# Performance work log

Hardware: AMD Instinct MI355X
Metric: run time of the kernel (lower is better)

Reference implementation:

```python
import jax, jax.numpy as jnp
import numpy as np

KS = 3        # kernel_size
DIL = 2       # dilation
HEAD_DIM = 32


def _unfold(x, ks, dil):
    """torch nn.Unfold(ks, dilation=dil, padding=dil*(ks-1)//2, stride=1).
    x: [B, C, H, W] -> [B, C, ks*ks, H, W] (channel-major patch order, matching torch)."""
    B, C, H, W = x.shape
    pad = dil * (ks - 1) // 2
    xp = jnp.pad(x, ((0, 0), (0, 0), (pad, pad), (pad, pad)))
    pats = [xp[:, :, i * dil:i * dil + H, j * dil:j * dil + W]
            for i in range(ks) for j in range(ks)]
    return jnp.stack(pats, axis=2)


def setup_inputs() -> dict:
    key = jax.random.key(0)
    k1, k2, k3 = jax.random.split(key, 3)
    shape = (16, 128, 64, 64)  # [B, d, H, W]
    return {
        "q": jax.random.normal(k1, shape, dtype=jnp.float32),
        "k": jax.random.normal(k2, shape, dtype=jnp.float32),
        "v": jax.random.normal(k3, shape, dtype=jnp.float32),
    }


def reference(q, k, v):
    B, d, H, W = q.shape
    heads = d // HEAD_DIM
    scale = HEAD_DIM ** (-0.5)
    KK = KS * KS
    # q: [B, heads, head_dim, H*W]
    qr = q.reshape(B, heads, HEAD_DIM, H * W)
    # unfolded k/v: [B, heads, head_dim, KK, H*W]
    ku = _unfold(k, KS, DIL).reshape(B, heads, HEAD_DIM, KK, H * W)
    vu = _unfold(v, KS, DIL).reshape(B, heads, HEAD_DIM, KK, H * W)
    # per-pixel small attention over KK local dilated keys
    attn = jnp.einsum('bhdn,bhdkn->bhnk', qr, ku) * scale  # [B,heads,HW,KK]
    attn = jax.nn.softmax(attn, axis=-1)  # attn_drop = 0 -> identity
    out = jnp.einsum('bhnk,bhdkn->bnhd', attn, vu)  # [B,HW,heads,head_dim]
    return out.reshape(B, H, W, d)
```

## Files before the change

### kernel.cpp

```cpp
#include <hip/hip_runtime.h>

namespace {
constexpr float SCALE = 0.17677669529663687f;
constexpr int CHP = 256;

typedef const __attribute__((address_space(1))) void gbl_v;
typedef __attribute__((address_space(3))) void lds_v;
typedef float v2f __attribute__((ext_vector_type(2)));

template<int CTRL>
__device__ __forceinline__ float qperm(float v) {
  return __builtin_bit_cast(float, __builtin_amdgcn_mov_dpp(
      __builtin_bit_cast(int, v), CTRL, 0xF, 0xF, true));
}

__global__ __launch_bounds__(512, 4) void dilate_attn(
    const float* __restrict__ q, const float* __restrict__ k,
    const float* __restrict__ v, float* __restrict__ out) {
  __shared__ float kbuf[32 * CHP];
  __shared__ float vbuf[32 * CHP];

  const int tid = threadIdx.x;
  const int cg  = tid & 7;
  const int pp  = (tid >> 3) & 31;
  const int rg  = tid >> 8;

  const int blk   = blockIdx.x;
  const int s     = blk >> 3;
  const int combo = ((blk & 7) << 3) | (s >> 5);
  const int pr    = s & 31;
  const int r0    = ((pr >> 1) << 2) | (pr & 1);
  const int b     = combo >> 2;
  const int head  = combo & 3;
  const int qrow  = r0 + 2 * rg;

  const size_t cb = ((size_t)b * 128 + head * 32) * 4096;
  const float* kp = k + cb;
  const float* vp = v + cb;

  int srow[4]; float vm[4];
  #pragma unroll
  for (int j = 0; j < 4; ++j) {
    const int ry = r0 - 2 + 2 * j;
    const bool ok = (unsigned)ry < 64u;
    srow[j] = (ok ? ry : r0) * 64;
    vm[j]   = ok ? 1.0f : 0.0f;
  }

  const int px0 = pp << 1;
  v2f q2[4];
  #pragma unroll
  for (int ci = 0; ci < 4; ++ci) {
    q2[ci] = *(const v2f*)(q + cb + (cg * 4 + ci) * 4096 + qrow * 64 + px0);
    q2[ci] *= SCALE;
  }

  int goff[4], loff[4];
  #pragma unroll
  for (int t = 0; t < 4; ++t) {
    const int l4  = t * 512 + tid;
    const int ch  = l4 >> 6;
    const int rem = l4 & 63;
    const int r   = rem >> 4;
    const int q4  = rem & 15;
    const int pxs = ((q4 - (ch >> 2)) & 15) << 2;
    goff[t] = ch * 4096 + srow[r] + pxs;
    loff[t] = l4 << 2;
  }
  #pragma unroll
  for (int t = 0; t < 4; ++t)
    __builtin_amdgcn_global_load_lds((gbl_v*)(kp + goff[t]), (lds_v*)(kbuf + loff[t]), 16, 0, 0);
  #pragma unroll
  for (int t = 0; t < 4; ++t)
    __builtin_amdgcn_global_load_lds((gbl_v*)(vp + goff[t]), (lds_v*)(vbuf + loff[t]), 16, 0, 0);

  asm volatile("s_waitcnt vmcnt(4)" ::: "memory");
  __builtin_amdgcn_s_barrier();
  asm volatile("" ::: "memory");

  const int   txL = (pp == 0)  ? 0  : px0 - 2;
  const int   txC = px0;
  const int   txR = (pp == 31) ? 62 : px0 + 2;
  const float mL  = (pp == 0)  ? 0.0f : 1.0f;
  const float mR  = (pp == 31) ? 0.0f : 1.0f;

  const int rot = cg << 2;
  const int tL  = (txL + rot) & 63;
  const int tC  = (txC + rot) & 63;
  const int tR  = (txR + rot) & 63;

  const int rbase = rg;

  v2f l[9];
  #pragma unroll
  for (int t = 0; t < 9; ++t) l[t] = (v2f)(0.0f);

  #pragma unroll
  for (int r = 0; r < 3; ++r) {
    #pragma unroll
    for (int ci = 0; ci < 4; ++ci) {
      const float* kc = kbuf + (cg * 4 + ci) * CHP + (rbase + r) * 64;
      const v2f kL = *(const v2f*)(kc + tL);
      const v2f kC = *(const v2f*)(kc + tC);
      const v2f kR = *(const v2f*)(kc + tR);
      l[r*3+0] = __builtin_elementwise_fma(q2[ci], kL, l[r*3+0]);
      l[r*3+1] = __builtin_elementwise_fma(q2[ci], kC, l[r*3+1]);
      l[r*3+2] = __builtin_elementwise_fma(q2[ci], kR, l[r*3+2]);
    }
  }

  asm volatile("s_waitcnt vmcnt(0)" ::: "memory");
  __builtin_amdgcn_s_barrier();
  asm volatile("" ::: "memory");

  v2f vr[3][4][3];
  #pragma unroll
  for (int r = 0; r < 3; ++r) {
    #pragma unroll
    for (int ci = 0; ci < 4; ++ci) {
      const float* vc = vbuf + (cg * 4 + ci) * CHP + (rbase + r) * 64;
      vr[r][ci][0] = *(const v2f*)(vc + tL);
      vr[r][ci][1] = *(const v2f*)(vc + tC);
      vr[r][ci][2] = *(const v2f*)(vc + tR);
    }
  }

  #pragma unroll
  for (int t = 0; t < 9; ++t) {
    l[t].x += qperm<0xB1>(l[t].x);
    l[t].y += qperm<0xB1>(l[t].y);
  }
  #pragma unroll
  for (int t = 0; t < 9; ++t) {
    l[t].x += qperm<0x4E>(l[t].x);
    l[t].y += qperm<0x4E>(l[t].y);
  }
  #pragma unroll
  for (int t = 0; t < 9; ++t) {
    l[t].x += __shfl_xor(l[t].x, 4, 64);
    l[t].y += __shfl_xor(l[t].y, 4, 64);
  }

  float msk[9];
  #pragma unroll
  for (int r = 0; r < 3; ++r) {
    msk[r*3+0] = vm[rbase + r] * mL;
    msk[r*3+1] = vm[rbase + r];
    msk[r*3+2] = vm[rbase + r] * mR;
  }
  v2f sum = (v2f)(0.0f);
  #pragma unroll
  for (int t = 0; t < 9; ++t) {
    l[t] *= msk[t];
    l[t].x = __expf(l[t].x);
    l[t].y = __expf(l[t].y);
    sum += l[t];
  }
  v2f rv; rv.x = 1.0f / sum.x; rv.y = 1.0f / sum.y;
  #pragma unroll
  for (int t = 0; t < 9; ++t)
    l[t] *= rv * msk[t];

  v2f o[4];
  #pragma unroll
  for (int ci = 0; ci < 4; ++ci) o[ci] = (v2f)(0.0f);
  #pragma unroll
  for (int r = 0; r < 3; ++r) {
    #pragma unroll
    for (int ci = 0; ci < 4; ++ci) {
      o[ci] = __builtin_elementwise_fma(l[r*3+0], vr[r][ci][0], o[ci]);
      o[ci] = __builtin_elementwise_fma(l[r*3+1], vr[r][ci][1], o[ci]);
      o[ci] = __builtin_elementwise_fma(l[r*3+2], vr[r][ci][2], o[ci]);
    }
  }

  float* ob = out + ((size_t)(b * 64 + qrow) * 64 + px0) * 128 + head * 32 + cg * 4;
  *(float4*)(ob)       = make_float4(o[0].x, o[1].x, o[2].x, o[3].x);
  *(float4*)(ob + 128) = make_float4(o[0].y, o[1].y, o[2].y, o[3].y);
}
}

extern "C" void kernel_launch(void* const* d_in, const int* in_sizes, int n_in,
                              void* d_out, int out_size, void* d_ws, size_t ws_size,
                              hipStream_t stream) {
  const float* q = (const float*)d_in[0];
  const float* k = (const float*)d_in[1];
  const float* v = (const float*)d_in[2];
  float* o = (float*)d_out;
  dilate_attn<<<dim3(2048), dim3(512), 0, stream>>>(q, k, v, o);
}
```

Before: 136.6 us.

## Process four row-pairs per block with a rolling K/V ring buffer

Each block now walks four consecutive output row tiles, using a 4-slot LDS ring for K and V rows. Each tile fetches only two new rows per tensor and reuses the overlapping halo rows, and prefetches for the next tile are issued during softmax and the V pass. This cuts redundant halo loads from global memory and reduces the grid from 2048 to 512 blocks. In exchange it adds extra barriers and serialises the work within each block, which lowers available parallelism on a GPU with many CUs.

```diff
diff --git a/kernel.cpp b/kernel.cpp
--- a/kernel.cpp
+++ b/kernel.cpp
@@ -2,7 +2,6 @@
 
 namespace {
 constexpr float SCALE = 0.17677669529663687f;
-constexpr int CHP = 256;
 
 typedef const __attribute__((address_space(1))) void gbl_v;
 typedef __attribute__((address_space(3))) void lds_v;
@@ -14,11 +13,15 @@
       __builtin_bit_cast(int, v), CTRL, 0xF, 0xF, true));
 }
 
+#define VMW0    asm volatile("s_waitcnt vmcnt(0)" ::: "memory")
+#define LKW0    asm volatile("s_waitcnt lgkmcnt(0)" ::: "memory")
+#define FENCE() asm volatile("" ::: "memory")
+
 __global__ __launch_bounds__(512, 4) void dilate_attn(
     const float* __restrict__ q, const float* __restrict__ k,
     const float* __restrict__ v, float* __restrict__ out) {
-  __shared__ float kbuf[32 * CHP];
-  __shared__ float vbuf[32 * CHP];
+  __shared__ float kbuf[4 * 2048];
+  __shared__ float vbuf[4 * 2048];
 
   const int tid = threadIdx.x;
   const int cg  = tid & 7;
@@ -26,157 +29,186 @@
   const int rg  = tid >> 8;
 
   const int blk   = blockIdx.x;
-  const int s     = blk >> 3;
-  const int combo = ((blk & 7) << 3) | (s >> 5);
-  const int pr    = s & 31;
-  const int r0    = ((pr >> 1) << 2) | (pr & 1);
+  const int xcd   = blk & 7;
+  const int m     = blk >> 3;
+  const int combo = (xcd << 3) | (m >> 3);
+  const int ck    = m & 7;
+  const int p     = ck >> 2;
+  const int c     = ck & 3;
+  const int R0    = p + (c << 4);
   const int b     = combo >> 2;
   const int head  = combo & 3;
-  const int qrow  = r0 + 2 * rg;
 
   const size_t cb = ((size_t)b * 128 + head * 32) * 4096;
   const float* kp = k + cb;
   const float* vp = v + cb;
-
-  int srow[4]; float vm[4];
-  #pragma unroll
-  for (int j = 0; j < 4; ++j) {
-    const int ry = r0 - 2 + 2 * j;
-    const bool ok = (unsigned)ry < 64u;
-    srow[j] = (ok ? ry : r0) * 64;
-    vm[j]   = ok ? 1.0f : 0.0f;
-  }
+  const float* qp = q + cb;
 
   const int px0 = pp << 1;
-  v2f q2[4];
-  #pragma unroll
-  for (int ci = 0; ci < 4; ++ci) {
-    q2[ci] = *(const v2f*)(q + cb + (cg * 4 + ci) * 4096 + qrow * 64 + px0);
-    q2[ci] *= SCALE;
-  }
-
-  int goff[4], loff[4];
-  #pragma unroll
-  for (int t = 0; t < 4; ++t) {
-    const int l4  = t * 512 + tid;
-    const int ch  = l4 >> 6;
-    const int rem = l4 & 63;
-    const int r   = rem >> 4;
-    const int q4  = rem & 15;
-    const int pxs = ((q4 - (ch >> 2)) & 15) << 2;
-    goff[t] = ch * 4096 + srow[r] + pxs;
-    loff[t] = l4 << 2;
-  }
-  #pragma unroll
-  for (int t = 0; t < 4; ++t)
-    __builtin_amdgcn_global_load_lds((gbl_v*)(kp + goff[t]), (lds_v*)(kbuf + loff[t]), 16, 0, 0);
-  #pragma unroll
-  for (int t = 0; t < 4; ++t)
-    __builtin_amdgcn_global_load_lds((gbl_v*)(vp + goff[t]), (lds_v*)(vbuf + loff[t]), 16, 0, 0);
-
-  asm volatile("s_waitcnt vmcnt(4)" ::: "memory");
-  __builtin_amdgcn_s_barrier();
-  asm volatile("" ::: "memory");
-
   const int   txL = (pp == 0)  ? 0  : px0 - 2;
   const int   txC = px0;
   const int   txR = (pp == 31) ? 62 : px0 + 2;
   const float mL  = (pp == 0)  ? 0.0f : 1.0f;
   const float mR  = (pp == 31) ? 0.0f : 1.0f;
-
   const int rot = cg << 2;
   const int tL  = (txL + rot) & 63;
   const int tC  = (txC + rot) & 63;
   const int tR  = (txR + rot) & 63;
 
-  const int rbase = rg;
-
-  v2f l[9];
-  #pragma unroll
-  for (int t = 0; t < 9; ++t) l[t] = (v2f)(0.0f);
-
-  #pragma unroll
-  for (int r = 0; r < 3; ++r) {
-    #pragma unroll
-    for (int ci = 0; ci < 4; ++ci) {
-      const float* kc = kbuf + (cg * 4 + ci) * CHP + (rbase + r) * 64;
-      const v2f kL = *(const v2f*)(kc + tL);
-      const v2f kC = *(const v2f*)(kc + tC);
-      const v2f kR = *(const v2f*)(kc + tR);
-      l[r*3+0] = __builtin_elementwise_fma(q2[ci], kL, l[r*3+0]);
-      l[r*3+1] = __builtin_elementwise_fma(q2[ci], kC, l[r*3+1]);
-      l[r*3+2] = __builtin_elementwise_fma(q2[ci], kR, l[r*3+2]);
-    }
-  }
-
-  asm volatile("s_waitcnt vmcnt(0)" ::: "memory");
-  __builtin_amdgcn_s_barrier();
-  asm volatile("" ::: "memory");
-
-  v2f vr[3][4][3];
-  #pragma unroll
-  for (int r = 0; r < 3; ++r) {
-    #pragma unroll
-    for (int ci = 0; ci < 4; ++ci) {
-      const float* vc = vbuf + (cg * 4 + ci) * CHP + (rbase + r) * 64;
-      vr[r][ci][0] = *(const v2f*)(vc + tL);
-      vr[r][ci][1] = *(const v2f*)(vc + tC);
-      vr[r][ci][2] = *(const v2f*)(vc + tR);
-    }
-  }
-
-  #pragma unroll
-  for (int t = 0; t < 9; ++t) {
-    l[t].x += qperm<0xB1>(l[t].x);
-    l[t].y += qperm<0xB1>(l[t].y);
-  }
-  #pragma unroll
-  for (int t = 0; t < 9; ++t) {
-    l[t].x += qperm<0x4E>(l[t].x);
-    l[t].y += qperm<0x4E>(l[t].y);
-  }
-  #pragma unroll
-  for (int t = 0; t < 9; ++t) {
-    l[t].x += __shfl_xor(l[t].x, 4, 64);
-    l[t].y += __shfl_xor(l[t].y, 4, 64);
-  }
-
-  float msk[9];
-  #pragma unroll
-  for (int r = 0; r < 3; ++r) {
-    msk[r*3+0] = vm[rbase + r] * mL;
-    msk[r*3+1] = vm[rbase + r];
-    msk[r*3+2] = vm[rbase + r] * mR;
-  }
-  v2f sum = (v2f)(0.0f);
-  #pragma unroll
-  for (int t = 0; t < 9; ++t) {
-    l[t] *= msk[t];
-    l[t].x = __expf(l[t].x);
-    l[t].y = __expf(l[t].y);
-    sum += l[t];
-  }
-  v2f rv; rv.x = 1.0f / sum.x; rv.y = 1.0f / sum.y;
-  #pragma unroll
-  for (int t = 0; t < 9; ++t)
-    l[t] *= rv * msk[t];
-
-  v2f o[4];
-  #pragma unroll
-  for (int ci = 0; ci < 4; ++ci) o[ci] = (v2f)(0.0f);
-  #pragma unroll
-  for (int r = 0; r < 3; ++r) {
-    #pragma unroll
-    for (int ci = 0; ci < 4; ++ci) {
-      o[ci] = __builtin_elementwise_fma(l[r*3+0], vr[r][ci][0], o[ci]);
-      o[ci] = __builtin_elementwise_fma(l[r*3+1], vr[r][ci][1], o[ci]);
-      o[ci] = __builtin_elementwise_fma(l[r*3+2], vr[r][ci][2], o[ci]);
-    }
-  }
-
-  float* ob = out + ((size_t)(b * 64 + qrow) * 64 + px0) * 128 + head * 32 + cg * 4;
-  *(float4*)(ob)       = make_float4(o[0].x, o[1].x, o[2].x, o[3].x);
-  *(float4*)(ob + 128) = make_float4(o[0].y, o[1].y, o[2].y, o[3].y);
+  #pragma unroll
+  for (int u = 0; u < 4; ++u) {
+    const int idx = u * 512 + tid;
+    const int sl  = idx >> 9;
+    const int ch  = (idx >> 4) & 31;
+    const int q4  = idx & 15;
+    int row = R0 - 2 + 2 * sl;
+    row = row < 0 ? 0 : row;
+    const int pxs = ((q4 - (ch >> 2)) & 15) << 2;
+    __builtin_amdgcn_global_load_lds((gbl_v*)(kp + ch * 4096 + row * 64 + pxs),
+                                     (lds_v*)(kbuf + (idx << 2)), 16, 0, 0);
+  }
+  FENCE();
+  v2f q2[4];
+  #pragma unroll
+  for (int ci = 0; ci < 4; ++ci) {
+    q2[ci] = *(const v2f*)(qp + (cg * 4 + ci) * 4096 + (R0 + 2 * rg) * 64 + px0);
+    q2[ci] *= SCALE;
+  }
+  FENCE();
+  #pragma unroll
+  for (int u = 0; u < 4; ++u) {
+    const int idx = u * 512 + tid;
+    const int sl  = idx >> 9;
+    const int ch  = (idx >> 4) & 31;
+    const int q4  = idx & 15;
+    int row = R0 - 2 + 2 * sl;
+    row = row < 0 ? 0 : row;
+    const int pxs = ((q4 - (ch >> 2)) & 15) << 2;
+    __builtin_amdgcn_global_load_lds((gbl_v*)(vp + ch * 4096 + row * 64 + pxs),
+                                     (lds_v*)(vbuf + (idx << 2)), 16, 0, 0);
+  }
+  FENCE();
+
+  #pragma unroll
+  for (int t = 0; t < 4; ++t) {
+    const int rt   = R0 + 4 * t;
+    const int qrow = rt + 2 * rg;
+
+    VMW0;
+    __builtin_amdgcn_s_barrier();
+    FENCE();
+
+    v2f l[9];
+    #pragma unroll
+    for (int i = 0; i < 9; ++i) l[i] = (v2f)(0.0f);
+    #pragma unroll
+    for (int r = 0; r < 3; ++r) {
+      const int slot = (2 * t + rg + r) & 3;
+      #pragma unroll
+      for (int ci = 0; ci < 4; ++ci) {
+        const float* kc = kbuf + slot * 2048 + (cg * 4 + ci) * 64;
+        l[r*3+0] = __builtin_elementwise_fma(q2[ci], *(const v2f*)(kc + tL), l[r*3+0]);
+        l[r*3+1] = __builtin_elementwise_fma(q2[ci], *(const v2f*)(kc + tC), l[r*3+1]);
+        l[r*3+2] = __builtin_elementwise_fma(q2[ci], *(const v2f*)(kc + tR), l[r*3+2]);
+      }
+    }
+
+    LKW0;
+    __builtin_amdgcn_s_barrier();
+    FENCE();
+    if (t < 3) {
+      const int s0 = (t & 1) << 1;
+      #pragma unroll
+      for (int u = 0; u < 2; ++u) {
+        const int idx = u * 512 + tid;
+        const int so  = idx >> 9;
+        const int ch  = (idx >> 4) & 31;
+        const int q4  = idx & 15;
+        int row = rt + 6 + 2 * so;
+        row = row > 63 ? 63 : row;
+        const int pxs = ((q4 - (ch >> 2)) & 15) << 2;
+        const int l4  = s0 * 512 + idx;
+        __builtin_amdgcn_global_load_lds((gbl_v*)(kp + ch * 4096 + row * 64 + pxs),
+                                         (lds_v*)(kbuf + (l4 << 2)), 16, 0, 0);
+      }
+      FENCE();
+    }
+
+    #pragma unroll
+    for (int i = 0; i < 9; ++i) { l[i].x += qperm<0xB1>(l[i].x); l[i].y += qperm<0xB1>(l[i].y); }
+    #pragma unroll
+    for (int i = 0; i < 9; ++i) { l[i].x += qperm<0x4E>(l[i].x); l[i].y += qperm<0x4E>(l[i].y); }
+    #pragma unroll
+    for (int i = 0; i < 9; ++i) {
+      l[i].x += __shfl_xor(l[i].x, 4, 64);
+      l[i].y += __shfl_xor(l[i].y, 4, 64);
+    }
+
+    float msk[9];
+    #pragma unroll
+    for (int r = 0; r < 3; ++r) {
+      const int row = qrow - 2 + 2 * r;
+      const float vmr = ((unsigned)row < 64u) ? 1.0f : 0.0f;
+      msk[r*3+0] = vmr * mL; msk[r*3+1] = vmr; msk[r*3+2] = vmr * mR;
+    }
+    v2f sum = (v2f)(0.0f);
+    #pragma unroll
+    for (int i = 0; i < 9; ++i) {
+      l[i] *= msk[i];
+      l[i].x = __expf(l[i].x);
+      l[i].y = __expf(l[i].y);
+      sum += l[i];
+    }
+    v2f rv; rv.x = 1.0f / sum.x; rv.y = 1.0f / sum.y;
+    #pragma unroll
+    for (int i = 0; i < 9; ++i) l[i] *= rv * msk[i];
+
+    v2f o[4];
+    #pragma unroll
+    for (int ci = 0; ci < 4; ++ci) o[ci] = (v2f)(0.0f);
+    #pragma unroll
+    for (int r = 0; r < 3; ++r) {
+      const int slot = (2 * t + rg + r) & 3;
+      #pragma unroll
+      for (int ci = 0; ci < 4; ++ci) {
+        const float* vc = vbuf + slot * 2048 + (cg * 4 + ci) * 64;
+        o[ci] = __builtin_elementwise_fma(l[r*3+0], *(const v2f*)(vc + tL), o[ci]);
+        o[ci] = __builtin_elementwise_fma(l[r*3+1], *(const v2f*)(vc + tC), o[ci]);
+        o[ci] = __builtin_elementwise_fma(l[r*3+2], *(const v2f*)(vc + tR), o[ci]);
+      }
+    }
+
+    float* ob = out + ((size_t)(b * 64 + qrow) * 64 + px0) * 128 + head * 32 + cg * 4;
+    *(float4*)(ob)       = make_float4(o[0].x, o[1].x, o[2].x, o[3].x);
+    *(float4*)(ob + 128) = make_float4(o[0].y, o[1].y, o[2].y, o[3].y);
+
+    if (t < 3) {
+      LKW0;
+      __builtin_amdgcn_s_barrier();
+      FENCE();
+      #pragma unroll
+      for (int ci = 0; ci < 4; ++ci) {
+        q2[ci] = *(const v2f*)(qp + (cg * 4 + ci) * 4096 + (qrow + 4) * 64 + px0);
+        q2[ci] *= SCALE;
+      }
+      FENCE();
+      const int s0 = (t & 1) << 1;
+      #pragma unroll
+      for (int u = 0; u < 2; ++u) {
+        const int idx = u * 512 + tid;
+        const int so  = idx >> 9;
+        const int ch  = (idx >> 4) & 31;
+        const int q4  = idx & 15;
+        int row = rt + 6 + 2 * so;
+        row = row > 63 ? 63 : row;
+        const int pxs = ((q4 - (ch >> 2)) & 15) << 2;
+        const int l4  = s0 * 512 + idx;
+        __builtin_amdgcn_global_load_lds((gbl_v*)(vp + ch * 4096 + row * 64 + pxs),
+                                         (lds_v*)(vbuf + (l4 << 2)), 16, 0, 0);
+      }
+      FENCE();
+    }
+  }
 }
 }
 
@@ -187,5 +219,5 @@
   const float* k = (const float*)d_in[1];
   const float* v = (const float*)d_in[2];
   float* o = (float*)d_out;
-  dilate_attn<<<dim3(2048), dim3(512), 0, stream>>>(q, k, v, o);
-}
+  dilate_attn<<<dim3(512), dim3(512), 0, stream>>>(q, k, v, o);
+}
```

Result: slower. 140.8 us (+3.1%).
